# Optimization experiments

Hardware: AMD Instinct MI355X
Metric: run time of the kernel (lower is better)

## Reference

```python
import jax, jax.numpy as jnp
import numpy as np
from jax import lax

H = 64          # num_heads
P = 64          # head_dim
N = 128         # ssm_state_size
G = 8           # n_groups
K = 4           # conv_kernel
D_MODEL = 4096  # hidden_size
I = H * P                      # intermediate_size = 4096
GN = G * N                     # groups_time_state_size = 1024
CONV_DIM = I + 2 * GN          # 6144
PROJ = I + CONV_DIM + H        # 10304
EPS = 1e-5
GROUP_SIZE = I // G            # 512


def setup_inputs() -> dict:
    key = jax.random.key(0)
    ks = jax.random.split(key, 6)
    B, L = 2, 2048
    s = 0.02
    return {
        "hidden_states": jax.random.normal(ks[0], (B, L, D_MODEL), jnp.float32),
        "in_proj_w": jax.random.normal(ks[1], (PROJ, D_MODEL), jnp.float32) * s,
        "conv_weight": jax.random.normal(ks[2], (CONV_DIM, K), jnp.float32) * s,
        "conv_bias": jnp.zeros((CONV_DIM,), jnp.float32),
        "dt_bias": jnp.ones((H,), jnp.float32),
        "A_log": jnp.log(jnp.arange(1, H + 1, dtype=jnp.float32)),
        "D": jnp.ones((H,), jnp.float32),
        "norm_weight": jnp.ones((I,), jnp.float32),
        "out_proj_w": jax.random.normal(ks[3], (D_MODEL, I), jnp.float32) * s,
    }


def reference(hidden_states, in_proj_w, conv_weight, conv_bias, dt_bias, A_log, D, norm_weight, out_proj_w):
    B, L, _ = hidden_states.shape

    # in_proj, then split into gate / conv-stream / dt
    proj = jnp.einsum("bld,pd->blp", hidden_states, in_proj_w)
    gate = proj[..., :I]
    hbc = proj[..., I:I + CONV_DIM]          # (B, L, conv_dim), pre-conv
    dt = proj[..., -H:]                       # (B, L, H)

    # depthwise causal conv1d + SiLU
    pad = jnp.pad(hbc, ((0, 0), (K - 1, 0), (0, 0)))
    conv = conv_bias
    for k in range(K):  # K=4, tiny fixed loop
        conv = conv + pad[:, k:k + L, :] * conv_weight[:, k]
    xBC = jax.nn.silu(conv)

    x = xBC[..., :I].reshape(B, L, H, P)                        # (B,L,H,P)
    Bm = xBC[..., I:I + GN].reshape(B, L, G, N)
    Cm = xBC[..., I + GN:].reshape(B, L, G, N)
    hpg = H // G
    B_h = jnp.repeat(Bm, hpg, axis=2)                            # (B,L,H,N)
    C_h = jnp.repeat(Cm, hpg, axis=2)                            # (B,L,H,N)

    # dt processing: softplus(dt + dt_bias), limits (0, inf)
    dt_p = jax.nn.softplus(dt + dt_bias)                         # (B,L,H)
    A = -jnp.exp(A_log)                                          # (H,)
    dA = jnp.exp(dt_p * A)                                       # (B,L,H)
    dtx = dt_p[..., None] * x                                    # (B,L,H,P)

    # selective scan over sequence (O(L)), state: (B,H,P,N)
    def step(state, inp):
        dA_t, dtx_t, B_t, C_t = inp
        state = state * dA_t[..., None, None] + dtx_t[..., None] * B_t[:, :, None, :]
        y_t = jnp.einsum("bhpn,bhn->bhp", state, C_t)
        return state, y_t

    xs = (jnp.moveaxis(dA, 1, 0), jnp.moveaxis(dtx, 1, 0),
          jnp.moveaxis(B_h, 1, 0), jnp.moveaxis(C_h, 1, 0))
    state0 = jnp.zeros((B, H, P, N), jnp.float32)
    final_state, ys = lax.scan(step, state0, xs)
    y = jnp.moveaxis(ys, 0, 1) + x * D[None, None, :, None]      # (B,L,H,P)
    y = y.reshape(B, L, I)

    # gated grouped RMSNorm: 8 independent RMSNorms over 512 elems each
    yg = y.reshape(B, L, G, GROUP_SIZE)
    var = jnp.mean(yg * yg, axis=-1, keepdims=True)
    yn = (yg * lax.rsqrt(var + EPS)).reshape(B, L, I) * norm_weight
    yn = yn * jax.nn.silu(gate)

    out = jnp.einsum("bli,di->bld", yn, out_proj_w)

    conv_state_new = jnp.moveaxis(hbc[:, L - (K - 1):, :], 1, 2)  # (B, conv_dim, K-1)
    return out, conv_state_new, final_state
```

## Files before the change

kernel.cpp:

```cpp
#include <hip/hip_runtime.h>
#include <cstdint>
#include <cstddef>

typedef __bf16 bf16;
typedef float f32x4 __attribute__((ext_vector_type(4)));
typedef bf16 bf16x8 __attribute__((ext_vector_type(8)));
typedef bf16 bf16x4 __attribute__((ext_vector_type(4)));

#define DM    4096
#define LL    2048
#define BB    2
#define BT    4096
#define II    4096
#define GN_   1024
#define CONVD 6144
#define PROJD 10304
#define NPAD  10496
#define HH    64
#define PP    64
#define NN    128
#define CT    64
#define NC    32

#define OUT_OFS_CONV  16777216
#define OUT_OFS_STATE 16814080

#define WS_HSB    0UL
#define WS_WINB   33554432UL
#define WS_DSB    0UL
#define WS_YNB    67108864UL
#define WS_PROJ   119537664UL
#define WS_XBC    205520896UL
#define WS_DTDA   255852544UL
#define WS_Y      257949696UL
#define WS_DTF    291504128UL
#define WS_HBC3   292552704UL
#define WS_WOUTB  292700160UL

__device__ __forceinline__ void gl2lds16(const void* g, void* l) {
  __builtin_amdgcn_global_load_lds(
      (__attribute__((address_space(1))) unsigned int*)(uintptr_t)g,
      (__attribute__((address_space(3))) unsigned int*)(uintptr_t)l, 16, 0, 0);
}

__global__ __launch_bounds__(256) void cast3_kernel(const float* __restrict__ s1,
                                                    bf16* __restrict__ d1,
                                                    const float* __restrict__ s2,
                                                    bf16* __restrict__ d2,
                                                    const float* __restrict__ s3,
                                                    bf16* __restrict__ d3,
                                                    long nsrc2, long ndst2) {
  const int bid = blockIdx.x;
  if (bid < 16384) {
    long i = ((long)bid * 256 + threadIdx.x) * 4;
    float4 v = *(const float4*)(s1 + i);
    bf16x4 o;
    o[0] = (bf16)v.x; o[1] = (bf16)v.y; o[2] = (bf16)v.z; o[3] = (bf16)v.w;
    *(bf16x4*)(d1 + i) = o;
  } else if (bid < 58368) {
    long i = ((long)(bid - 16384) * 256 + threadIdx.x) * 4;
    if (i >= ndst2) return;
    bf16x4 o;
    if (i < nsrc2) {
      float4 v = *(const float4*)(s2 + i);
      o[0] = (bf16)v.x; o[1] = (bf16)v.y; o[2] = (bf16)v.z; o[3] = (bf16)v.w;
    } else {
      o[0] = (bf16)0.f; o[1] = (bf16)0.f; o[2] = (bf16)0.f; o[3] = (bf16)0.f;
    }
    *(bf16x4*)(d2 + i) = o;
  } else {
    long i = ((long)(bid - 58368) * 256 + threadIdx.x) * 4;
    float4 v = *(const float4*)(s3 + i);
    bf16x4 o;
    o[0] = (bf16)v.x; o[1] = (bf16)v.y; o[2] = (bf16)v.z; o[3] = (bf16)v.w;
    *(bf16x4*)(d3 + i) = o;
  }
}

#define BARF() do { asm volatile("" ::: "memory");                    \
                    __builtin_amdgcn_s_barrier();                     \
                    asm volatile("" ::: "memory"); } while (0)
#define WAITLGKM0() do { asm volatile("s_waitcnt lgkmcnt(0)" ::: "memory"); \
                         __builtin_amdgcn_sched_barrier(0); } while (0)
#define HINTLGKM8() asm volatile("s_waitcnt lgkmcnt(8)" ::: "memory")
#define WAITVM(n) asm volatile("s_waitcnt vmcnt(" #n ")" ::: "memory")
#define PRIO1 __builtin_amdgcn_s_setprio(1)
#define PRIO0 __builtin_amdgcn_s_setprio(0)

__device__ __forceinline__ void stage_A_half(const bf16* __restrict__ A, int K,
                                             int arow, int kt, bf16* lds,
                                             int h, int tid) {
#pragma unroll
  for (int j = 0; j < 2; ++j) {
    const int r  = h * 64 + j * 128 + (tid >> 3);
    const int cb = (tid & 7) * 16;
    const int cs = cb ^ ((r & 7) << 4);
    gl2lds16(A + (size_t)(arow + r) * K + kt * 64 + (cs >> 1),
             lds + r * 64 + (cb >> 1));
  }
}
__device__ __forceinline__ void stage_B_half(const bf16* __restrict__ B, int K,
                                             int brow, int kt, bf16* lds,
                                             int h, int tid) {
#pragma unroll
  for (int j = 0; j < 2; ++j) {
    const int quarter = j * 2 + (tid >> 8);
    const int kq = tid & 255;
    const int r  = quarter * 64 + h * 32 + (kq >> 3);
    const int cb = (kq & 7) * 16;
    const int cs = cb ^ ((r & 7) << 4);
    gl2lds16(B + (size_t)(brow + r) * K + kt * 64 + (cs >> 1),
             lds + r * 64 + (cb >> 1));
  }
}

#define LDA4(p, mh) do {                                                     \
  _Pragma("unroll") for (int mt = 0; mt < 4; ++mt)                           \
  _Pragma("unroll") for (int kk = 0; kk < 2; ++kk) {                         \
    const int rr = wm * 128 + (mh) * 64 + mt * 16 + l16;                     \
    const int cc = (kk * 64 + quad * 16) ^ ((rr & 7) << 4);                  \
    a_[mt][kk] = *(const bf16x8*)((const char*)(&sA[p][rr][0]) + cc);        \
  } } while (0)

#define LDB2(p, np, barr) do {                                               \
  _Pragma("unroll") for (int nt = 0; nt < 2; ++nt)                           \
  _Pragma("unroll") for (int kk = 0; kk < 2; ++kk) {                         \
    const int rr = wn * 64 + (np) * 32 + nt * 16 + l16;                      \
    const int cc = (kk * 64 + quad * 16) ^ ((rr & 7) << 4);                  \
    barr[nt][kk] = *(const bf16x8*)((const char*)(&sB[p][rr][0]) + cc);      \
  } } while (0)

#define MFMAQ(mh, barr, nb0) do {                                            \
  _Pragma("unroll") for (int kk = 0; kk < 2; ++kk)                           \
  _Pragma("unroll") for (int mt = 0; mt < 4; ++mt)                           \
  _Pragma("unroll") for (int nt = 0; nt < 2; ++nt)                           \
    acc[(mh) * 4 + mt][(nb0) + nt] = __builtin_amdgcn_mfma_f32_16x16x32_bf16(\
        a_[mt][kk], barr[nt][kk], acc[(mh) * 4 + mt][(nb0) + nt], 0, 0, 0);  \
  } while (0)

template <int MODE>
__global__ __launch_bounds__(512, 2) void gemm256(const bf16* __restrict__ A,
                                                  const bf16* __restrict__ B,
                                                  void* __restrict__ Cv,
                                                  int M, int N, int K, int NB,
                                                  float* __restrict__ dtf,
                                                  float* __restrict__ hbc3) {
  __shared__ __align__(16) bf16 sA[2][256][64];
  __shared__ __align__(16) bf16 sB[2][256][64];

  const int tid  = threadIdx.x;
  const int wave = tid >> 6, lane = tid & 63;
  const int l16  = lane & 15, quad = lane >> 4;
  const int wm   = wave >> 2, wn = wave & 3;

  const int nwg = gridDim.x;
  const int q = nwg >> 3, r8 = nwg & 7;
  const int xcd = blockIdx.x & 7, idx = blockIdx.x >> 3;
  const int wgid = (xcd < r8 ? xcd * (q + 1) : r8 * (q + 1) + (xcd - r8) * q) + idx;
  const int mb = wgid / NB, nb = wgid - mb * NB;
  const int arow = mb * 256, brow = nb * 256;

  f32x4 acc[8][4];
#pragma unroll
  for (int i = 0; i < 8; ++i)
#pragma unroll
    for (int j = 0; j < 4; ++j) acc[i][j] = (f32x4)0.f;

  const int NT = K >> 6;

  stage_A_half(A, K, arow, 0, &sA[0][0][0], 0, tid);
  stage_B_half(B, K, brow, 0, &sB[0][0][0], 0, tid);
  stage_A_half(A, K, arow, 0, &sA[0][0][0], 1, tid);
  stage_B_half(B, K, brow, 0, &sB[0][0][0], 1, tid);
  stage_A_half(A, K, arow, 1, &sA[1][0][0], 0, tid);
  stage_B_half(B, K, brow, 1, &sB[1][0][0], 0, tid);
  stage_A_half(A, K, arow, 1, &sA[1][0][0], 1, tid);
  WAITVM(6);
  BARF();

  bf16x8 a_[4][2], b0_[2][2], b1_[2][2];

  for (int i = 0; i < NT / 2; ++i) {
    const int t1o = 2 * i + 1;
    const int t2  = (2 * i + 2 < NT) ? 2 * i + 2 : NT - 1;
    const int t3  = (2 * i + 3 < NT) ? 2 * i + 3 : NT - 1;

    LDA4(0, 0); LDB2(0, 0, b0_);
    stage_B_half(B, K, brow, t1o, &sB[1][0][0], 1, tid);
    HINTLGKM8();
    BARF(); WAITLGKM0();
    PRIO1; MFMAQ(0, b0_, 0); PRIO0;
    BARF();
    LDB2(0, 1, b1_);
    stage_A_half(A, K, arow, t2, &sA[0][0][0], 0, tid);
    BARF(); WAITLGKM0();
    PRIO1; MFMAQ(0, b1_, 2); PRIO0;
    BARF();
    LDA4(0, 1);
    stage_B_half(B, K, brow, t2, &sB[0][0][0], 0, tid);
    BARF(); WAITLGKM0();
    PRIO1; MFMAQ(1, b1_, 2); PRIO0;
    BARF();
    stage_A_half(A, K, arow, t2, &sA[0][0][0], 1, tid);
    WAITVM(6);
    BARF();
    PRIO1; MFMAQ(1, b0_, 0); PRIO0;
    BARF();
    LDA4(1, 0); LDB2(1, 0, b0_);
    stage_B_half(B, K, brow, t2, &sB[0][0][0], 1, tid);
    HINTLGKM8();
    BARF(); WAITLGKM0();
    PRIO1; MFMAQ(0, b0_, 0); PRIO0;
    BARF();
    LDB2(1, 1, b1_);
    stage_A_half(A, K, arow, t3, &sA[1][0][0], 0, tid);
    BARF(); WAITLGKM0();
    PRIO1; MFMAQ(0, b1_, 2); PRIO0;
    BARF();
    LDA4(1, 1);
    stage_B_half(B, K, brow, t3, &sB[1][0][0], 0, tid);
    BARF(); WAITLGKM0();
    PRIO1; MFMAQ(1, b1_, 2); PRIO0;
    BARF();
    stage_A_half(A, K, arow, t3, &sA[1][0][0], 1, tid);
    WAITVM(6);
    BARF();
    PRIO1; MFMAQ(1, b0_, 0); PRIO0;
    BARF();
  }
  asm volatile("s_waitcnt vmcnt(0)" ::: "memory");
  __builtin_amdgcn_s_barrier();

#pragma unroll
  for (int mt = 0; mt < 8; ++mt) {
    const int row0 = arow + wm * 128 + mt * 16 + quad * 4;
#pragma unroll
    for (int nt = 0; nt < 4; ++nt) {
      const int col = brow + wn * 64 + nt * 16 + l16;
#pragma unroll
      for (int r = 0; r < 4; ++r) {
        const float v = acc[mt][nt][r];
        const int row = row0 + r;
        if constexpr (MODE == 0) {
          ((float*)Cv)[(size_t)row * N + col] = v;
        } else {
          ((bf16*)Cv)[(size_t)row * N + col] = (bf16)v;
          const int dc = col - (II + CONVD);
          if (dc >= 0 && dc < 64) dtf[(size_t)row * 64 + dc] = v;
          const int rr = row & (LL - 1);
          if (rr >= LL - 3 && col >= II && col < II + CONVD)
            hbc3[((size_t)(row >> 11) * 3 + (rr - (LL - 3))) * CONVD + (col - II)] = v;
        }
      }
    }
  }
}

#define CTILE 64
__global__ __launch_bounds__(256) void conv_kernel(const bf16* __restrict__ proj,
                                                   const float* __restrict__ cw,
                                                   const float* __restrict__ cb,
                                                   bf16* __restrict__ xbc) {
  const int c   = blockIdx.x * 256 + threadIdx.x;
  const int bt0 = blockIdx.y * CTILE;
  const int t0  = bt0 & (LL - 1);
  const float4 w = *(const float4*)(cw + c * 4);
  const float bias = cb[c];
  const bf16* p = proj + (size_t)bt0 * NPAD + II + c;
  float h0, h1, h2;
  if (t0 == 0) {
    h0 = 0.f; h1 = 0.f; h2 = 0.f;
  } else {
    h0 = (float)p[-3 * (ptrdiff_t)NPAD];
    h1 = (float)p[-2 * (ptrdiff_t)NPAD];
    h2 = (float)p[-(ptrdiff_t)NPAD];
  }
  bf16* q = xbc + (size_t)bt0 * CONVD + c;
#pragma unroll 8
  for (int t = 0; t < CTILE; ++t) {
    const float cur = (float)p[(ptrdiff_t)t * NPAD];
    const float acc = bias + h0 * w.x + h1 * w.y + h2 * w.z + cur * w.w;
    q[(size_t)t * CONVD] = (bf16)(acc / (1.f + __expf(-acc)));
    h0 = h1; h1 = h2; h2 = cur;
  }
}

__global__ __launch_bounds__(256) void dtcs_kernel(const float* __restrict__ dtf,
                                                   const float* __restrict__ hbc3,
                                                   const float* __restrict__ dt_bias,
                                                   const float* __restrict__ A_log,
                                                   float* __restrict__ dtda,
                                                   float* __restrict__ outp) {
  const int bid = blockIdx.x;
  if (bid < 1024) {
    const int idx = bid * 256 + threadIdx.x;
    const int h = idx & 63;
    const float z = dtf[idx] + dt_bias[h];
    const float sp = (z > 20.f) ? z : log1pf(__expf(z));
    const float a = -__expf(A_log[h]);
    float2 o; o.x = sp; o.y = __expf(sp * a);
    *(float2*)(dtda + (size_t)idx * 2) = o;
  } else {
    const int idx = (bid - 1024) * 256 + threadIdx.x;
    if (idx >= BB * CONVD * 3) return;
    const int b = idx / (CONVD * 3);
    const int r = idx - b * CONVD * 3;
    const int c = r / 3, j = r - c * 3;
    outp[idx] = hbc3[((size_t)b * 3 + j) * CONVD + c];
  }
}

#define SCAN_DECODE()                                                  \
  const int lin = blockIdx.x;                                          \
  const int hh  = (lin >> 3) & 7;                                      \
  const int id  = (lin & 7) | ((lin >> 6) << 3);                       \
  const int g   = id >> 6, c = (id >> 1) & 31, b = id & 1;             \
  const int h   = g * 8 + hh;

__global__ __launch_bounds__(256) void chunkA_kernel(const bf16* __restrict__ xbc,
                                                     const float* __restrict__ dtda,
                                                     const float* __restrict__ A_log,
                                                     bf16* __restrict__ ybuf,
                                                     bf16* __restrict__ dsb) {
  SCAN_DECODE();
  const int tid = threadIdx.x;
  const int wave = tid >> 6, lane = tid & 63;
  const int l16 = lane & 15, quad = lane >> 4;

  __shared__ __align__(16) bf16 CsBt[8192];
  __shared__ __align__(16) bf16 Bs[64][128];
  __shared__ __align__(16) bf16 Xt[64][64];
  __shared__ __align__(16) bf16 Ws[64][64];
  __shared__ float cums[64], dtps[64], wls[64];

  bf16 (*Cs)[128] = (bf16(*)[128])CsBt;
  bf16 (*Bt)[64]  = (bf16(*)[64])CsBt;

  const size_t rowbase = ((size_t)b * LL + (size_t)c * CT) * CONVD;

  {
    const int r0 = wave * 16;
    const bf16* gC = xbc + rowbase + (II + GN_) + g * 128;
    const bf16* gB = xbc + rowbase + II + g * 128;
#pragma unroll
    for (int j = 0; j < 4; ++j) {
      const int r  = r0 + j * 4 + (lane >> 4);
      const int ch = (lane & 15) ^ (r & 15);
      gl2lds16(gC + (size_t)r * CONVD + ch * 8, &Cs[r0 + j * 4][0]);
      gl2lds16(gB + (size_t)r * CONVD + ch * 8, &Bs[r0 + j * 4][0]);
    }
  }
  {
    const int j = tid >> 2, p0 = (tid & 3) * 16;
    const bf16* gpX = xbc + rowbase + (size_t)j * CONVD + h * 64 + p0;
#pragma unroll
    for (int k = 0; k < 2; ++k) {
      bf16x8 v = *(const bf16x8*)(gpX + k * 8);
#pragma unroll
      for (int e = 0; e < 8; ++e) {
        const int pp = p0 + k * 8 + e;
        Xt[pp][(((j >> 3) ^ (pp & 7)) * 8) + (j & 7)] = v[e];
      }
    }
  }
  if (wave == 0) {
    const float Ah = -__expf(A_log[h]);
    float2 dd = *(const float2*)(dtda + ((size_t)((b * LL + c * CT + lane)) * 64 + h) * 2);
    float s = dd.x * Ah;
#pragma unroll
    for (int d = 1; d < 64; d <<= 1) {
      float v = __shfl_up(s, d);
      if (lane >= d) s += v;
    }
    const float tot = __shfl(s, 63);
    cums[lane] = s;
    dtps[lane] = dd.x;
    wls[lane]  = __expf(tot - s) * dd.x;
  }
  __syncthreads();

  const int mrow = wave * 16 + l16;
  {
    f32x4 accg[4];
#pragma unroll
    for (int nt = 0; nt < 4; ++nt) accg[nt] = (f32x4)0.f;
#pragma unroll
    for (int k0 = 0; k0 < 128; k0 += 32) {
      bf16x8 af = *(const bf16x8*)&Cs[mrow][(((k0 >> 3) + quad) ^ (mrow & 15)) * 8];
#pragma unroll
      for (int nt = 0; nt < 4; ++nt) {
        const int nrow = nt * 16 + l16;
        bf16x8 bfr = *(const bf16x8*)&Bs[nrow][(((k0 >> 3) + quad) ^ (nrow & 15)) * 8];
        accg[nt] = __builtin_amdgcn_mfma_f32_16x16x32_bf16(af, bfr, accg[nt], 0, 0, 0);
      }
    }
#pragma unroll
    for (int nt = 0; nt < 4; ++nt) {
      const int j = nt * 16 + l16;
#pragma unroll
      for (int r = 0; r < 4; ++r) {
        const int i = wave * 16 + quad * 4 + r;
        float v = 0.f;
        if (j <= i) v = accg[nt][r] * __expf(cums[i] - cums[j]) * dtps[j];
        Ws[i][(((j >> 3) ^ (i & 7)) * 8) + (j & 7)] = (bf16)v;
      }
    }
  }
  __syncthreads();

  {
    const int n = tid >> 1, j0 = (tid & 1) * 32;
#pragma unroll
    for (int k = 0; k < 4; ++k) {
      bf16x8 v;
#pragma unroll
      for (int e = 0; e < 8; ++e) {
        const int j = j0 + k * 8 + e;
        v[e] = Bs[j][(((n >> 3) ^ (j & 15)) * 8) + (n & 7)];
      }
      *(bf16x8*)(&Bt[n][((((j0 + k * 8) >> 3) ^ (n & 7)) * 8)]) = v;
    }
  }
  __syncthreads();

  f32x4 accy[4];
#pragma unroll
  for (int pt = 0; pt < 4; ++pt) accy[pt] = (f32x4)0.f;
#pragma unroll
  for (int k0 = 0; k0 < 64; k0 += 32) {
    bf16x8 af = *(const bf16x8*)&Ws[mrow][(((k0 >> 3) + quad) ^ (mrow & 7)) * 8];
#pragma unroll
    for (int pt = 0; pt < 4; ++pt) {
      const int prow = pt * 16 + l16;
      bf16x8 bfr = *(const bf16x8*)&Xt[prow][(((k0 >> 3) + quad) ^ (prow & 7)) * 8];
      accy[pt] = __builtin_amdgcn_mfma_f32_16x16x32_bf16(af, bfr, accy[pt], 0, 0, 0);
    }
  }

  f32x4 accs[8];
#pragma unroll
  for (int nt = 0; nt < 8; ++nt) accs[nt] = (f32x4)0.f;
#pragma unroll
  for (int k0 = 0; k0 < 64; k0 += 32) {
    bf16x8 axr = *(const bf16x8*)&Xt[mrow][(((k0 >> 3) + quad) ^ (mrow & 7)) * 8];
    bf16x8 ax;
#pragma unroll
    for (int e = 0; e < 8; ++e)
      ax[e] = (bf16)((float)axr[e] * wls[k0 + quad * 8 + e]);
#pragma unroll
    for (int nt = 0; nt < 8; ++nt) {
      const int nrow = nt * 16 + l16;
      bf16x8 bfr = *(const bf16x8*)&Bt[nrow][(((k0 >> 3) + quad) ^ (nrow & 7)) * 8];
      accs[nt] = __builtin_amdgcn_mfma_f32_16x16x32_bf16(ax, bfr, accs[nt], 0, 0, 0);
    }
  }

#pragma unroll
  for (int pt = 0; pt < 4; ++pt) {
#pragma unroll
    for (int r = 0; r < 4; ++r) {
      const int i = wave * 16 + quad * 4 + r;
      ybuf[((size_t)(b * LL + c * CT + i)) * II + h * 64 + pt * 16 + l16] = (bf16)accy[pt][r];
    }
  }
  const size_t dbase = (((size_t)(b * HH + h)) * NC + c) * (CT * NN);
#pragma unroll
  for (int nt = 0; nt < 8; ++nt) {
#pragma unroll
    for (int r = 0; r < 4; ++r) {
      const int p = wave * 16 + quad * 4 + r;
      dsb[dbase + (size_t)p * NN + nt * 16 + l16] = (bf16)accs[nt][r];
    }
  }
}

__global__ __launch_bounds__(256) void chain_kernel(const float* __restrict__ dtda,
                                                    const float* __restrict__ A_log,
                                                    bf16* __restrict__ dsb,
                                                    float* __restrict__ fst) {
  const int blk = blockIdx.x;
  const int b = blk >> 8, h = (blk >> 2) & 63, qtr = blk & 3;
  const int tid = threadIdx.x, wave = tid >> 6, lane = tid & 63;
  __shared__ float DcL[NC];

  const float Ah = -__expf(A_log[h]);
#pragma unroll
  for (int cc = 0; cc < 8; ++cc) {
    const int c = wave * 8 + cc;
    float2 dd = *(const float2*)(dtda + ((size_t)(b * LL + c * CT + lane) * 64 + h) * 2);
    float a = dd.x * Ah;
#pragma unroll
    for (int m = 1; m <= 32; m <<= 1) a += __shfl_xor(a, m);
    if (lane == 0) DcL[c] = __expf(a);
  }

  const int local = qtr * 2048 + tid * 8;
  const size_t base = ((size_t)(b * HH + h)) * NC * (CT * NN) + local;
  float s[8];
#pragma unroll
  for (int e = 0; e < 8; ++e) s[e] = 0.f;

  bf16x8 d0 = *(const bf16x8*)(dsb + base);
  __syncthreads();

  for (int c = 0; c < NC; ++c) {
    bf16* p = dsb + base + (size_t)c * (CT * NN);
    bf16x8 dn;
    if (c + 1 < NC) dn = *(const bf16x8*)(p + (CT * NN));
    const float dc = DcL[c];
    bf16x8 o0;
#pragma unroll
    for (int e = 0; e < 8; ++e) o0[e] = (bf16)s[e];
    *(bf16x8*)(p) = o0;
#pragma unroll
    for (int e = 0; e < 8; ++e) s[e] = s[e] * dc + (float)d0[e];
    d0 = dn;
  }
  float* fp = fst + ((size_t)(b * HH + h)) * (PP * NN) + local;
#pragma unroll
  for (int k = 0; k < 2; ++k) {
    float4 v = { s[k * 4], s[k * 4 + 1], s[k * 4 + 2], s[k * 4 + 3] };
    *(float4*)(fp + k * 4) = v;
  }
}

__global__ __launch_bounds__(512) void chunkBN_kernel(const bf16* __restrict__ xbc,
                                                      const float* __restrict__ dtda,
                                                      const float* __restrict__ A_log,
                                                      const float* __restrict__ Dv,
                                                      const bf16* __restrict__ spb,
                                                      const bf16* __restrict__ ybi,
                                                      const bf16* __restrict__ proj,
                                                      const float* __restrict__ nw,
                                                      bf16* __restrict__ ynb) {
  const int lin = blockIdx.x;
  const int g = lin >> 6, c = (lin >> 1) & 31, b = lin & 1;
  const int tid = threadIdx.x;
  const int w = tid >> 6, lane = tid & 63;
  const int l16 = lane & 15, quad = lane >> 4;
  const int h = g * 8 + w;

  __shared__ __align__(16) char LB[147456];
  __shared__ float sums[8][64];
  __shared__ float es[64];
  __shared__ float rstd[64];

  bf16 (*Cs)[128] = (bf16(*)[128])LB;
  bf16 (*Sp)[128] = (bf16(*)[128])(LB + 16384 + (size_t)w * 16384);

  const size_t rowbase = ((size_t)b * LL + (size_t)c * CT) * CONVD;
  {
    const bf16* gC = xbc + rowbase + (II + GN_) + g * 128;
#pragma unroll
    for (int j = 0; j < 2; ++j) {
      const int r  = w * 8 + j * 4 + (lane >> 4);
      const int ch = (lane & 15) ^ (r & 15);
      gl2lds16(gC + (size_t)r * CONVD + ch * 8, LB + (w * 8 + j * 4) * 256);
    }
    const bf16* gS = spb + (((size_t)(b * HH + h)) * NC + c) * (CT * NN);
#pragma unroll
    for (int j = 0; j < 16; ++j) {
      const int r  = j * 4 + (lane >> 4);
      const int ch = (lane & 15) ^ (r & 15);
      gl2lds16(gS + (size_t)r * NN + ch * 8, LB + 16384 + w * 16384 + j * 1024);
    }
  }
  if (w == 0) {
    const float Ah = -__expf(A_log[h]);
  }
  __shared__ float esw[8][64];
  {
    const float Ah = -__expf(A_log[h]);
    float2 dd = *(const float2*)(dtda + ((size_t)(b * LL + c * CT + lane) * 64 + h) * 2);
    float s = dd.x * Ah;
#pragma unroll
    for (int d = 1; d < 64; d <<= 1) {
      float v = __shfl_up(s, d);
      if (lane >= d) s += v;
    }
    esw[w][lane] = __expf(s);
  }
  __syncthreads();

  f32x4 acc[4][4];
#pragma unroll
  for (int it = 0; it < 4; ++it)
#pragma unroll
    for (int pt = 0; pt < 4; ++pt) acc[it][pt] = (f32x4)0.f;

#pragma unroll
  for (int k0 = 0; k0 < 128; k0 += 32) {
    bf16x8 af[4], bfr[4];
#pragma unroll
    for (int it = 0; it < 4; ++it) {
      const int rr = it * 16 + l16;
      af[it]  = *(const bf16x8*)&Cs[rr][(((k0 >> 3) + quad) ^ (rr & 15)) * 8];
      bfr[it] = *(const bf16x8*)&Sp[rr][(((k0 >> 3) + quad) ^ (rr & 15)) * 8];
    }
#pragma unroll
    for (int it = 0; it < 4; ++it)
#pragma unroll
      for (int pt = 0; pt < 4; ++pt)
        acc[it][pt] = __builtin_amdgcn_mfma_f32_16x16x32_bf16(af[it], bfr[pt], acc[it][pt], 0, 0, 0);
  }

  const float Dh = Dv[h];
  const size_t grow0 = (size_t)b * LL + (size_t)c * CT;
#pragma unroll
  for (int it = 0; it < 4; ++it)
#pragma unroll
    for (int pt = 0; pt < 4; ++pt)
#pragma unroll
      for (int r = 0; r < 4; ++r) {
        const int row = it * 16 + quad * 4 + r;
        const int colh = pt * 16 + l16;
        const size_t gr = grow0 + row;
        acc[it][pt][r] = acc[it][pt][r] * esw[w][row]
                       + (float)ybi[gr * II + h * 64 + colh]
                       + Dh * (float)xbc[gr * CONVD + h * 64 + colh];
      }

  float ssv[4][4];
#pragma unroll
  for (int it = 0; it < 4; ++it)
#pragma unroll
    for (int r = 0; r < 4; ++r) {
      float s = 0.f;
#pragma unroll
      for (int pt = 0; pt < 4; ++pt) s += acc[it][pt][r] * acc[it][pt][r];
#pragma unroll
      for (int m = 1; m <= 8; m <<= 1) s += __shfl_xor(s, m);
      ssv[it][r] = s;
    }
  if (l16 == 0) {
#pragma unroll
    for (int it = 0; it < 4; ++it)
#pragma unroll
      for (int r = 0; r < 4; ++r)
        sums[w][it * 16 + quad * 4 + r] = ssv[it][r];
  }
  __syncthreads();

  if (tid < 64) {
    float tot = 0.f;
#pragma unroll
    for (int ww = 0; ww < 8; ++ww) tot += sums[ww][tid];
    rstd[tid] = rsqrtf(tot * (1.f / 512.f) + 1e-5f);
  }
  float* yls = (float*)LB;
#pragma unroll
  for (int it = 0; it < 4; ++it)
#pragma unroll
    for (int pt = 0; pt < 4; ++pt)
#pragma unroll
      for (int r = 0; r < 4; ++r)
        yls[(it * 16 + quad * 4 + r) * 516 + w * 64 + pt * 16 + l16] = acc[it][pt][r];
  __syncthreads();

  {
    const int row = tid >> 3, ch = tid & 7;
    const size_t gr = grow0 + row;
    const float rs = rstd[row];
#pragma unroll
    for (int k = 0; k < 4; ++k) {
      const int col = ch * 16 + k * 128;
      const float* yl = yls + (size_t)row * 516 + col;
      bf16x8 gv0 = *(const bf16x8*)(proj + gr * NPAD + g * 512 + col);
      bf16x8 gv1 = *(const bf16x8*)(proj + gr * NPAD + g * 512 + col + 8);
      bf16x8 o0, o1;
#pragma unroll
      for (int e = 0; e < 8; ++e) {
        const float gf0 = (float)gv0[e];
        const float gf1 = (float)gv1[e];
        const float v0 = yl[e]     * rs * nw[g * 512 + col + e]     * (gf0 / (1.f + __expf(-gf0)));
        const float v1 = yl[e + 8] * rs * nw[g * 512 + col + e + 8] * (gf1 / (1.f + __expf(-gf1)));
        o0[e] = (bf16)v0; o1[e] = (bf16)v1;
      }
      *(bf16x8*)(ynb + gr * II + g * 512 + col)     = o0;
      *(bf16x8*)(ynb + gr * II + g * 512 + col + 8) = o1;
    }
  }
}

extern "C" void kernel_launch(void* const* d_in, const int* in_sizes, int n_in,
                              void* d_out, int out_size, void* d_ws, size_t ws_size,
                              hipStream_t stream) {
  const float* hs      = (const float*)d_in[0];
  const float* w_in    = (const float*)d_in[1];
  const float* cw      = (const float*)d_in[2];
  const float* cb      = (const float*)d_in[3];
  const float* dt_bias = (const float*)d_in[4];
  const float* A_log   = (const float*)d_in[5];
  const float* Dv      = (const float*)d_in[6];
  const float* nw      = (const float*)d_in[7];
  const float* w_out   = (const float*)d_in[8];

  char* ws = (char*)d_ws;
  bf16*  hsb   = (bf16*)(ws + WS_HSB);
  bf16*  winb  = (bf16*)(ws + WS_WINB);
  bf16*  dsb   = (bf16*)(ws + WS_DSB);
  bf16*  ynb   = (bf16*)(ws + WS_YNB);
  bf16*  proj  = (bf16*)(ws + WS_PROJ);
  bf16*  xbc   = (bf16*)(ws + WS_XBC);
  float* dtda  = (float*)(ws + WS_DTDA);
  bf16*  ybuf  = (bf16*)(ws + WS_Y);
  float* dtf   = (float*)(ws + WS_DTF);
  float* hbc3  = (float*)(ws + WS_HBC3);
  bf16*  woutb = (bf16*)(ws + WS_WOUTB);

  float* outp = (float*)d_out;

  cast3_kernel<<<74752, 256, 0, stream>>>(hs, hsb, w_in, winb, w_out, woutb,
                                          (long)PROJD * DM, (long)NPAD * DM);

  gemm256<1><<<(BT / 256) * (NPAD / 256), 512, 0, stream>>>(
      hsb, winb, proj, BT, NPAD, DM, NPAD / 256, dtf, hbc3);

  conv_kernel<<<dim3(CONVD / 256, BT / CTILE), 256, 0, stream>>>(proj, cw, cb, xbc);
  dtcs_kernel<<<1168, 256, 0, stream>>>(dtf, hbc3, dt_bias, A_log, dtda, outp + OUT_OFS_CONV);

  chunkA_kernel<<<4096, 256, 0, stream>>>(xbc, dtda, A_log, ybuf, dsb);
  chain_kernel<<<BB * HH * 4, 256, 0, stream>>>(dtda, A_log, dsb, outp + OUT_OFS_STATE);
  chunkBN_kernel<<<512, 512, 0, stream>>>(xbc, dtda, A_log, Dv, dsb, ybuf, proj, nw, ynb);

  gemm256<0><<<(BT / 256) * (DM / 256), 512, 0, stream>>>(
      ynb, woutb, outp, BT, DM, II, DM / 256, nullptr, nullptr);
}
```

Before: 906.4 us.

## Precompute GEMM staging pointers, column-major tile order, hoist epilogue side-writes

Staging addresses for the A and B tiles are computed once per block and kept in registers instead of being rebuilt at every stage. The block-to-tile mapping now walks 16 M-tiles per N column (mb = wgid & 15), so consecutive blocks share the same weight tile, which should improve L2 reuse of the large weight matrix. The per-element dt and conv-state side writes are moved out of the main epilogue into block-uniform branches, which removes per-element compares from every block. The risks are the extra registers needed for the precomputed pointers, and the hard-coded 16 M-tiles, which assumes BT/256 == 16.

Result: no change. 920.5 us (+1.6%).

```diff
diff --git a/kernel.cpp b/kernel.cpp
--- a/kernel.cpp
+++ b/kernel.cpp
@@ -87,32 +87,12 @@
 #define PRIO1 __builtin_amdgcn_s_setprio(1)
 #define PRIO0 __builtin_amdgcn_s_setprio(0)
 
-__device__ __forceinline__ void stage_A_half(const bf16* __restrict__ A, int K,
-                                             int arow, int kt, bf16* lds,
-                                             int h, int tid) {
-#pragma unroll
-  for (int j = 0; j < 2; ++j) {
-    const int r  = h * 64 + j * 128 + (tid >> 3);
-    const int cb = (tid & 7) * 16;
-    const int cs = cb ^ ((r & 7) << 4);
-    gl2lds16(A + (size_t)(arow + r) * K + kt * 64 + (cs >> 1),
-             lds + r * 64 + (cb >> 1));
-  }
-}
-__device__ __forceinline__ void stage_B_half(const bf16* __restrict__ B, int K,
-                                             int brow, int kt, bf16* lds,
-                                             int h, int tid) {
-#pragma unroll
-  for (int j = 0; j < 2; ++j) {
-    const int quarter = j * 2 + (tid >> 8);
-    const int kq = tid & 255;
-    const int r  = quarter * 64 + h * 32 + (kq >> 3);
-    const int cb = (kq & 7) * 16;
-    const int cs = cb ^ ((r & 7) << 4);
-    gl2lds16(B + (size_t)(brow + r) * K + kt * 64 + (cs >> 1),
-             lds + r * 64 + (cb >> 1));
-  }
-}
+#define STA(p, kt, h) do {                                                   \
+  gl2lds16(pA[h][0] + (size_t)(kt) * 64, &sA[p][0][0] + loA[h][0]);          \
+  gl2lds16(pA[h][1] + (size_t)(kt) * 64, &sA[p][0][0] + loA[h][1]); } while (0)
+#define STB(p, kt, h) do {                                                   \
+  gl2lds16(pB[h][0] + (size_t)(kt) * 64, &sB[p][0][0] + loB[h][0]);          \
+  gl2lds16(pB[h][1] + (size_t)(kt) * 64, &sB[p][0][0] + loB[h][1]); } while (0)
 
 #define LDA4(p, mh) do {                                                     \
   _Pragma("unroll") for (int mt = 0; mt < 4; ++mt)                           \
@@ -142,7 +122,7 @@
 __global__ __launch_bounds__(512, 2) void gemm256(const bf16* __restrict__ A,
                                                   const bf16* __restrict__ B,
                                                   void* __restrict__ Cv,
-                                                  int M, int N, int K, int NB,
+                                                  int M, int N, int K,
                                                   float* __restrict__ dtf,
                                                   float* __restrict__ hbc3) {
   __shared__ __align__(16) bf16 sA[2][256][64];
@@ -157,9 +137,33 @@
   const int q = nwg >> 3, r8 = nwg & 7;
   const int xcd = blockIdx.x & 7, idx = blockIdx.x >> 3;
   const int wgid = (xcd < r8 ? xcd * (q + 1) : r8 * (q + 1) + (xcd - r8) * q) + idx;
-  const int mb = wgid / NB, nb = wgid - mb * NB;
+  const int mb = wgid & 15, nb = wgid >> 4;
   const int arow = mb * 256, brow = nb * 256;
 
+  const bf16 *pA[2][2], *pB[2][2];
+  int loA[2][2], loB[2][2];
+#pragma unroll
+  for (int h = 0; h < 2; ++h)
+#pragma unroll
+    for (int j = 0; j < 2; ++j) {
+      {
+        const int r  = h * 64 + j * 128 + (tid >> 3);
+        const int cb = (tid & 7) * 16;
+        const int cs = cb ^ ((r & 7) << 4);
+        pA[h][j]  = A + (size_t)(arow + r) * K + (cs >> 1);
+        loA[h][j] = r * 64 + (cb >> 1);
+      }
+      {
+        const int quarter = j * 2 + (tid >> 8);
+        const int kq = tid & 255;
+        const int r  = quarter * 64 + h * 32 + (kq >> 3);
+        const int cb = (kq & 7) * 16;
+        const int cs = cb ^ ((r & 7) << 4);
+        pB[h][j]  = B + (size_t)(brow + r) * K + (cs >> 1);
+        loB[h][j] = r * 64 + (cb >> 1);
+      }
+    }
+
   f32x4 acc[8][4];
 #pragma unroll
   for (int i = 0; i < 8; ++i)
@@ -168,13 +172,13 @@
 
   const int NT = K >> 6;
 
-  stage_A_half(A, K, arow, 0, &sA[0][0][0], 0, tid);
-  stage_B_half(B, K, brow, 0, &sB[0][0][0], 0, tid);
-  stage_A_half(A, K, arow, 0, &sA[0][0][0], 1, tid);
-  stage_B_half(B, K, brow, 0, &sB[0][0][0], 1, tid);
-  stage_A_half(A, K, arow, 1, &sA[1][0][0], 0, tid);
-  stage_B_half(B, K, brow, 1, &sB[1][0][0], 0, tid);
-  stage_A_half(A, K, arow, 1, &sA[1][0][0], 1, tid);
+  STA(0, 0, 0);
+  STB(0, 0, 0);
+  STA(0, 0, 1);
+  STB(0, 0, 1);
+  STA(1, 1, 0);
+  STB(1, 1, 0);
+  STA(1, 1, 1);
   WAITVM(6);
   BARF();
 
@@ -186,43 +190,43 @@
     const int t3  = (2 * i + 3 < NT) ? 2 * i + 3 : NT - 1;
 
     LDA4(0, 0); LDB2(0, 0, b0_);
-    stage_B_half(B, K, brow, t1o, &sB[1][0][0], 1, tid);
+    STB(1, t1o, 1);
     HINTLGKM8();
     BARF(); WAITLGKM0();
     PRIO1; MFMAQ(0, b0_, 0); PRIO0;
     BARF();
     LDB2(0, 1, b1_);
-    stage_A_half(A, K, arow, t2, &sA[0][0][0], 0, tid);
+    STA(0, t2, 0);
     BARF(); WAITLGKM0();
     PRIO1; MFMAQ(0, b1_, 2); PRIO0;
     BARF();
     LDA4(0, 1);
-    stage_B_half(B, K, brow, t2, &sB[0][0][0], 0, tid);
+    STB(0, t2, 0);
     BARF(); WAITLGKM0();
     PRIO1; MFMAQ(1, b1_, 2); PRIO0;
     BARF();
-    stage_A_half(A, K, arow, t2, &sA[0][0][0], 1, tid);
+    STA(0, t2, 1);
     WAITVM(6);
     BARF();
     PRIO1; MFMAQ(1, b0_, 0); PRIO0;
     BARF();
     LDA4(1, 0); LDB2(1, 0, b0_);
-    stage_B_half(B, K, brow, t2, &sB[0][0][0], 1, tid);
+    STB(0, t2, 1);
     HINTLGKM8();
     BARF(); WAITLGKM0();
     PRIO1; MFMAQ(0, b0_, 0); PRIO0;
     BARF();
     LDB2(1, 1, b1_);
-    stage_A_half(A, K, arow, t3, &sA[1][0][0], 0, tid);
+    STA(1, t3, 0);
     BARF(); WAITLGKM0();
     PRIO1; MFMAQ(0, b1_, 2); PRIO0;
     BARF();
     LDA4(1, 1);
-    stage_B_half(B, K, brow, t3, &sB[1][0][0], 0, tid);
+    STB(1, t3, 0);
     BARF(); WAITLGKM0();
     PRIO1; MFMAQ(1, b1_, 2); PRIO0;
     BARF();
-    stage_A_half(A, K, arow, t3, &sA[1][0][0], 1, tid);
+    STA(1, t3, 1);
     WAITVM(6);
     BARF();
     PRIO1; MFMAQ(1, b0_, 0); PRIO0;
@@ -240,16 +244,42 @@
 #pragma unroll
       for (int r = 0; r < 4; ++r) {
         const float v = acc[mt][nt][r];
-        const int row = row0 + r;
         if constexpr (MODE == 0) {
-          ((float*)Cv)[(size_t)row * N + col] = v;
+          ((float*)Cv)[(size_t)(row0 + r) * N + col] = v;
         } else {
-          ((bf16*)Cv)[(size_t)row * N + col] = (bf16)v;
-          const int dc = col - (II + CONVD);
-          if (dc >= 0 && dc < 64) dtf[(size_t)row * 64 + dc] = v;
-          const int rr = row & (LL - 1);
-          if (rr >= LL - 3 && col >= II && col < II + CONVD)
-            hbc3[((size_t)(row >> 11) * 3 + (rr - (LL - 3))) * CONVD + (col - II)] = v;
+          ((bf16*)Cv)[(size_t)(row0 + r) * N + col] = (bf16)v;
+        }
+      }
+    }
+  }
+  if constexpr (MODE == 1) {
+    if (brow == II + CONVD && wn == 0) {
+#pragma unroll
+      for (int mt = 0; mt < 8; ++mt) {
+        const int row0 = arow + wm * 128 + mt * 16 + quad * 4;
+#pragma unroll
+        for (int nt = 0; nt < 4; ++nt) {
+          const int dc = nt * 16 + l16;
+#pragma unroll
+          for (int r = 0; r < 4; ++r)
+            dtf[(size_t)(row0 + r) * 64 + dc] = acc[mt][nt][r];
+        }
+      }
+    }
+    if (brow >= II && brow < II + CONVD && (arow & (LL - 1)) == LL - 256) {
+#pragma unroll
+      for (int mt = 0; mt < 8; ++mt) {
+        const int row0 = arow + wm * 128 + mt * 16 + quad * 4;
+#pragma unroll
+        for (int nt = 0; nt < 4; ++nt) {
+          const int col = brow + wn * 64 + nt * 16 + l16;
+#pragma unroll
+          for (int r = 0; r < 4; ++r) {
+            const int row = row0 + r;
+            const int rr = row & (LL - 1);
+            if (rr >= LL - 3)
+              hbc3[((size_t)(row >> 11) * 3 + (rr - (LL - 3))) * CONVD + (col - II)] = acc[mt][nt][r];
+          }
         }
       }
     }
@@ -542,8 +572,8 @@
 
   __shared__ __align__(16) char LB[147456];
   __shared__ float sums[8][64];
-  __shared__ float es[64];
   __shared__ float rstd[64];
+  __shared__ float esw[8][64];
 
   bf16 (*Cs)[128] = (bf16(*)[128])LB;
   bf16 (*Sp)[128] = (bf16(*)[128])(LB + 16384 + (size_t)w * 16384);
@@ -565,10 +595,6 @@
       gl2lds16(gS + (size_t)r * NN + ch * 8, LB + 16384 + w * 16384 + j * 1024);
     }
   }
-  if (w == 0) {
-    const float Ah = -__expf(A_log[h]);
-  }
-  __shared__ float esw[8][64];
   {
     const float Ah = -__expf(A_log[h]);
     float2 dd = *(const float2*)(dtda + ((size_t)(b * LL + c * CT + lane) * 64 + h) * 2);
@@ -714,7 +740,7 @@
                                           (long)PROJD * DM, (long)NPAD * DM);
 
   gemm256<1><<<(BT / 256) * (NPAD / 256), 512, 0, stream>>>(
-      hsb, winb, proj, BT, NPAD, DM, NPAD / 256, dtf, hbc3);
+      hsb, winb, proj, BT, NPAD, DM, dtf, hbc3);
 
   conv_kernel<<<dim3(CONVD / 256, BT / CTILE), 256, 0, stream>>>(proj, cw, cb, xbc);
   dtcs_kernel<<<1168, 256, 0, stream>>>(dtf, hbc3, dt_bias, A_log, dtda, outp + OUT_OFS_CONV);
@@ -724,5 +750,5 @@
   chunkBN_kernel<<<512, 512, 0, stream>>>(xbc, dtda, A_log, Dv, dsb, ybuf, proj, nw, ynb);
 
   gemm256<0><<<(BT / 256) * (DM / 256), 512, 0, stream>>>(
-      ynb, woutb, outp, BT, DM, II, DM / 256, nullptr, nullptr);
-}
+      ynb, woutb, outp, BT, DM, II, nullptr, nullptr);
+}
```
